# Optimization experiments

Measured on AMD Instinct MI355X. Metric: run time of the kernel, lower is better.

The kernel has to match this reference:

```python
import jax, jax.numpy as jnp
import numpy as np

F_IN = 128
HID = 256
OUT = 64
E = 500_000
NP_ALL = 304_096   # paper nodes: seed 4096 + hop1 100000 + hop2 200000
NP_H01 = 104_096   # paper nodes kept at layer 1 (seed + hop1)
NA_ALL = 154_096   # author nodes: 4096 + 50000 + 100000
NA_H01 = 54_096    # author nodes kept at layer 1


def setup_inputs() -> dict:
    key = jax.random.key(0)
    ks = iter(jax.random.split(key, 40))
    def nrm(shape, scale=0.05):
        return jax.random.normal(next(ks), shape, dtype=jnp.float32) * scale
    inp = {
        'x_paper': nrm((NP_ALL, F_IN), 1.0),
        'x_author': nrm((NA_ALL, F_IN), 1.0),
    }
    # per-layer, per-edge-type SAGEConv params: lin_l (W,b on aggregated msgs), lin_r (W, no bias, on dst)
    for li, fin in ((0, F_IN), (1, HID)):
        for rel in ('cites', 'writes', 'rev'):
            inp[f'l{li}_{rel}_Wl'] = nrm((fin, HID))
            inp[f'l{li}_{rel}_b'] = jnp.zeros((HID,), jnp.float32)
            inp[f'l{li}_{rel}_Wr'] = nrm((fin, HID))
    inp['lin_W'] = nrm((HID, OUT))
    inp['lin_b'] = jnp.zeros((OUT,), jnp.float32)
    # edge_index per edge type per sampled hop; hop-1 edges survive trimming at layer 1
    for name, hi in (('e_cites_h1', NP_H01), ('e_cites_h2', NP_ALL),
                     ('e_writes_h1', NA_H01), ('e_writes_h2', NA_ALL),
                     ('e_rev_h1', NA_H01), ('e_rev_h2', NA_ALL)):
        inp[name] = jax.random.randint(next(ks), (2, E), 0, hi, dtype=jnp.int32)
    return inp


def _sage(x_src, x_dst, edge, Wl, b, Wr):
    # SAGEConv: mean-aggregate neighbor features, lin_l(agg) + b + lin_r(x_dst)
    n_dst = x_dst.shape[0]
    msg = x_src[edge[0]]  # [E, F] gather
    s = jax.ops.segment_sum(msg, edge[1], num_segments=n_dst)
    cnt = jax.ops.segment_sum(jnp.ones((edge.shape[1],), x_src.dtype), edge[1], num_segments=n_dst)
    mean = s / jnp.maximum(cnt, 1.0)[:, None]  # 0 for isolated dst nodes (PyG mean)
    return mean @ Wl + b + x_dst @ Wr


def reference(x_paper, x_author,
              l0_cites_Wl, l0_cites_b, l0_cites_Wr,
              l0_writes_Wl, l0_writes_b, l0_writes_Wr,
              l0_rev_Wl, l0_rev_b, l0_rev_Wr,
              l1_cites_Wl, l1_cites_b, l1_cites_Wr,
              l1_writes_Wl, l1_writes_b, l1_writes_Wr,
              l1_rev_Wl, l1_rev_b, l1_rev_Wr,
              lin_W, lin_b,
              e_cites_h1, e_cites_h2, e_writes_h1, e_writes_h2, e_rev_h1, e_rev_h2):
    # ---- layer 0: no trimming -> all nodes, all (hop1+hop2) edges ----
    ec = jnp.concatenate([e_cites_h1, e_cites_h2], axis=1)
    ew = jnp.concatenate([e_writes_h1, e_writes_h2], axis=1)
    er = jnp.concatenate([e_rev_h1, e_rev_h2], axis=1)
    p = _sage(x_paper, x_paper, ec, l0_cites_Wl, l0_cites_b, l0_cites_Wr) \
      + _sage(x_author, x_paper, ew, l0_writes_Wl, l0_writes_b, l0_writes_Wr)
    a = _sage(x_paper, x_author, er, l0_rev_Wl, l0_rev_b, l0_rev_Wr)
    xp, xa = jax.nn.relu(p), jax.nn.relu(a)
    # ---- layer 1: trim_to_layer drops last hop nodes + hop-2 edges ----
    xp, xa = xp[:NP_H01], xa[:NA_H01]
    p = _sage(xp, xp, e_cites_h1, l1_cites_Wl, l1_cites_b, l1_cites_Wr) \
      + _sage(xa, xp, e_writes_h1, l1_writes_Wl, l1_writes_b, l1_writes_Wr)
    xp = jax.nn.relu(p)
    # final Linear on 'paper' features
    return xp @ lin_W + lin_b
```

## Files before the change

kernel.cpp:

```cpp
#include <hip/hip_runtime.h>

typedef unsigned short u16;
typedef unsigned int   u32;
typedef __bf16  bf16x8 __attribute__((ext_vector_type(8)));
typedef float   floatx4 __attribute__((ext_vector_type(4)));

#define NP_ALL 304096
#define NP_H01 104096
#define NA_ALL 154096
#define NA_H01 54096

#define SEG_C0 0
#define SEG_W0 104096
#define SEG_R0 208192
#define SEG_C1 262288
#define SEG_W1 366384
#define SCAN_N 470480
#define SCAN_NBLK 1838

__device__ __forceinline__ u16 f2bf(float f){
    u32 u = __float_as_uint(f);
    return (u16)((u + 0x7fffu + ((u>>16)&1u)) >> 16);
}
__device__ __forceinline__ float blo(u32 v){ return __uint_as_float(v<<16); }
__device__ __forceinline__ float bhi(u32 v){ return __uint_as_float(v & 0xFFFF0000u); }

__global__ void wcvt_k(u16* __restrict__ dst, const float* __restrict__ src, int n){
    int t = blockIdx.x*256 + threadIdx.x;
    if (t < n) dst[t] = f2bf(src[t]);
}
__global__ void wadd_k(u16* __restrict__ dst, const float* __restrict__ a, const float* __restrict__ b, int n){
    int t = blockIdx.x*256 + threadIdx.x;
    if (t < n) dst[t] = f2bf(a[t] + b[t]);
}
__global__ void bias_k(float* __restrict__ dst, const float* __restrict__ a, const float* __restrict__ b, int n){
    int t = blockIdx.x*256 + threadIdx.x;
    if (t < n) dst[t] = a[t] + (b ? b[t] : 0.0f);
}
__global__ void cvt2_k(u32* __restrict__ dst, const float* __restrict__ src, int n2){
    int t = blockIdx.x*256 + threadIdx.x;
    if (t >= n2) return;
    dst[t] = (u32)f2bf(src[2*t]) | ((u32)f2bf(src[2*t+1])<<16);
}
__global__ void repack_k(const u16* __restrict__ Wc, int K, int N, u16* __restrict__ Wp){
    int t = blockIdx.x*256 + threadIdx.x;
    int total = (K>>5)*(N>>4)*64;
    if (t >= total) return;
    int lane = t & 63;
    int nt = (t>>6) % (N>>4);
    int kt = (t>>6) / (N>>4);
    int n  = nt*16 + (lane & 15);
    int k0 = kt*32 + (lane>>4)*8;
    u16* dst = Wp + (size_t)t*8;
    #pragma unroll
    for (int j=0;j<8;j++) dst[j] = Wc[(size_t)(k0+j)*N + n];
}

__global__ void hist_k(const int* __restrict__ edst, int nE, int limit, int* __restrict__ deg){
    int t = blockIdx.x*256 + threadIdx.x;
    if (t >= nE) return;
    int d = edst[t];
    if (d < limit) atomicAdd(deg + d, 1);
}
__global__ void scan1_k(const int* __restrict__ deg, int* __restrict__ bsum){
    __shared__ int sm[256];
    int t = blockIdx.x*256 + threadIdx.x;
    sm[threadIdx.x] = (t < SCAN_N) ? deg[t] : 0;
    __syncthreads();
    for (int s=128; s>0; s>>=1){
        if (threadIdx.x < s) sm[threadIdx.x] += sm[threadIdx.x+s];
        __syncthreads();
    }
    if (threadIdx.x == 0) bsum[blockIdx.x] = sm[0];
}
__global__ void scan2_k(int* __restrict__ bsum, int n){
    __shared__ int sm[256];
    int chunk = (n + 255) >> 8;
    int st = threadIdx.x * chunk;
    int sum = 0;
    for (int i=0;i<chunk;i++){ int idx = st+i; if (idx < n) sum += bsum[idx]; }
    sm[threadIdx.x] = sum; __syncthreads();
    int acc = sum;
    for (int s=1; s<256; s<<=1){
        int t2 = (threadIdx.x >= s) ? sm[threadIdx.x - s] : 0;
        __syncthreads();
        acc += t2; sm[threadIdx.x] = acc;
        __syncthreads();
    }
    int excl = acc - sum;
    for (int i=0;i<chunk;i++){
        int idx = st+i;
        if (idx < n){ int v = bsum[idx]; bsum[idx] = excl; excl += v; }
    }
}
__global__ void scan3_k(const int* __restrict__ deg, const int* __restrict__ bsum,
                        int* __restrict__ rowptr, int* __restrict__ wp){
    __shared__ int sm[256];
    int t = blockIdx.x*256 + threadIdx.x;
    int v = (t < SCAN_N) ? deg[t] : 0;
    sm[threadIdx.x] = v; __syncthreads();
    int acc = v;
    for (int s=1; s<256; s<<=1){
        int t2 = (threadIdx.x >= s) ? sm[threadIdx.x - s] : 0;
        __syncthreads();
        acc += t2; sm[threadIdx.x] = acc;
        __syncthreads();
    }
    int excl = acc - v + bsum[blockIdx.x];
    if (t < SCAN_N){ rowptr[t] = excl; wp[t] = excl; }
    if (t == SCAN_N-1) rowptr[SCAN_N] = excl + v;
}
__global__ void fill_k(const int* __restrict__ esrc, const int* __restrict__ edst,
                       int nE, int limit, int* __restrict__ wp, int* __restrict__ pool){
    int t = blockIdx.x*256 + threadIdx.x;
    if (t >= nE) return;
    int d = edst[t];
    if (d >= limit) return;
    int p = atomicAdd(wp + d, 1);
    pool[p] = esrc[t];
}

template<int D>
__device__ __forceinline__ void gather_mean(
    const u16* __restrict__ srcl, size_t rstride,
    const int* __restrict__ rowptr, int seg, int d,
    const int* __restrict__ pool, u16* __restrict__ outl)
{
    int b = rowptr[seg + d], e = rowptr[seg + d + 1];
    float rc = 1.0f / (float)((e - b) > 1 ? (e - b) : 1);
    if (D == 128) {
        float a0=0,a1=0,c0=0,c1=0;
        int i = b;
        for (; i+1 < e; i += 2){
            int s0 = pool[i], s1 = pool[i+1];
            u32 v0 = *(const u32*)(srcl + (size_t)s0*rstride);
            u32 v1 = *(const u32*)(srcl + (size_t)s1*rstride);
            a0 += blo(v0); a1 += bhi(v0);
            c0 += blo(v1); c1 += bhi(v1);
        }
        if (i < e){
            int s0 = pool[i];
            u32 v0 = *(const u32*)(srcl + (size_t)s0*rstride);
            a0 += blo(v0); a1 += bhi(v0);
        }
        u32 lo = f2bf((a0+c0)*rc), hi = f2bf((a1+c1)*rc);
        *(u32*)outl = lo | (hi<<16);
    } else {
        float a0=0,a1=0,a2=0,a3=0,c0=0,c1=0,c2=0,c3=0;
        int i = b;
        for (; i+1 < e; i += 2){
            int s0 = pool[i], s1 = pool[i+1];
            uint2 v0 = *(const uint2*)(srcl + (size_t)s0*rstride);
            uint2 v1 = *(const uint2*)(srcl + (size_t)s1*rstride);
            a0 += blo(v0.x); a1 += bhi(v0.x); a2 += blo(v0.y); a3 += bhi(v0.y);
            c0 += blo(v1.x); c1 += bhi(v1.x); c2 += blo(v1.y); c3 += bhi(v1.y);
        }
        if (i < e){
            int s0 = pool[i];
            uint2 v0 = *(const uint2*)(srcl + (size_t)s0*rstride);
            a0 += blo(v0.x); a1 += bhi(v0.x); a2 += blo(v0.y); a3 += bhi(v0.y);
        }
        uint2 o;
        o.x = (u32)f2bf((a0+c0)*rc) | ((u32)f2bf((a1+c1)*rc)<<16);
        o.y = (u32)f2bf((a2+c2)*rc) | ((u32)f2bf((a3+c3)*rc)<<16);
        *(uint2*)outl = o;
    }
}


__global__ __launch_bounds__(256) void gAp_k(
    const u16* __restrict__ xpb, const u16* __restrict__ xab,
    const int* __restrict__ rowptr, const int* __restrict__ pool,
    u16* __restrict__ Ap)
{
    int gid = blockIdx.x*256 + threadIdx.x;
    int wid = gid >> 6, lane = gid & 63;
    if (wid >= NP_H01) return;
    const size_t SM = (size_t)NP_H01*64;
    size_t wofs = (size_t)wid*64 + 2*(lane&31);
    int hs = lane>>5;
    gather_mean<128>(xpb + 2*lane, 128, rowptr, SEG_C0, wid, pool, Ap + (size_t)(0+hs)*SM + wofs);
    gather_mean<128>(xab + 2*lane, 128, rowptr, SEG_W0, wid, pool, Ap + (size_t)(2+hs)*SM + wofs);
    u32 v = *(const u32*)(xpb + (size_t)wid*128 + 2*lane);
    *(u32*)(Ap + (size_t)(4+hs)*SM + wofs) = v;
}
__global__ __launch_bounds__(256) void gAa_k(
    const u16* __restrict__ xpb, const u16* __restrict__ xab,
    const int* __restrict__ rowptr, const int* __restrict__ pool,
    u16* __restrict__ Aa)
{
    int gid = blockIdx.x*256 + threadIdx.x;
    int wid = gid >> 6, lane = gid & 63;
    if (wid >= NA_H01) return;
    const size_t SM = (size_t)NA_H01*64;
    size_t wofs = (size_t)wid*64 + 2*(lane&31);
    int hs = lane>>5;
    gather_mean<128>(xpb + 2*lane, 128, rowptr, SEG_R0, wid, pool, Aa + (size_t)(0+hs)*SM + wofs);
    u32 v = *(const u32*)(xab + (size_t)wid*128 + 2*lane);
    *(u32*)(Aa + (size_t)(2+hs)*SM + wofs) = v;
}
__global__ __launch_bounds__(256) void gA1_k(
    const u16* __restrict__ A1src,
    const u16* __restrict__ xa,
    const int* __restrict__ rowptr, const int* __restrict__ pool,
    u16* __restrict__ A1)
{
    int gid = blockIdx.x*256 + threadIdx.x;
    int wid = gid >> 6, lane = gid & 63;
    if (wid >= NP_H01) return;
    const size_t SM = (size_t)NP_H01*64;
    int qs = lane>>4;
    size_t wofs = (size_t)wid*64 + 4*(lane&15);
    gather_mean<256>(A1src + (size_t)(8+qs)*SM + 4*(lane&15), 64,
                     rowptr, SEG_C1, wid, pool, A1 + (size_t)(0+qs)*SM + wofs);
    gather_mean<256>(xa + 4*lane, 256,
                     rowptr, SEG_W1, wid, pool, A1 + (size_t)(4+qs)*SM + wofs);
}

template<int WROWS, int WCOLS, int WMT, int WNT, bool RELU, bool F32OUT>
__global__ __launch_bounds__(256, 2) void gemm4_k(
    const u16* __restrict__ At, int M, int K,
    const u16* __restrict__ Wp, int nt16, const float* __restrict__ bias,
    void* __restrict__ C_, int ldc, int tileM, int colofs)
{
    constexpr int BNT  = WCOLS*WNT;
    constexpr int BM   = WROWS*WMT*16;
    constexpr int NSTG = 2*BNT;
    constexpr int PERW = NSTG/4;
    static_assert(2*WMT == 8, "vmcnt(8) literal assumes 8 A-loads per stage");
    __shared__ __align__(16) u16 ldsB[2*NSTG*512];

    int wave = threadIdx.x >> 6, lane = threadIdx.x & 63;
    int quad = lane >> 4, l15 = lane & 15;
    int wr = wave / WCOLS, wc = wave % WCOLS;
    int bm0 = blockIdx.x * BM;
    int ntb = blockIdx.y * BNT;
    const size_t SMS = (size_t)M*64;

    floatx4 acc[WMT][WNT];
    #pragma unroll
    for (int i=0;i<WMT;i++)
        #pragma unroll
        for (int j=0;j<WNT;j++) acc[i][j] = (floatx4){0.f,0.f,0.f,0.f};

    const u16* Abase[WMT];
    #pragma unroll
    for (int i=0;i<WMT;i++){
        int r = bm0 + (wr*WMT + i)*16 + l15;
        r = (r < M) ? r : (M-1);
        Abase[i] = At + (size_t)r*64 + quad*8;
    }

    int nstages = K >> 6;

    auto stage_issue = [&](int sn, int bufsel){
        #pragma unroll
        for (int i=0;i<PERW;i++){
            int g = wave*PERW + i;
            int ktl = g / BNT, ntl = g % BNT;
            const u16* gp = Wp + ((size_t)(sn*2+ktl)*nt16 + ntb + ntl)*512 + lane*8;
            u16* lp = ldsB + bufsel*(NSTG*512) + g*512 + lane*8;
            __builtin_amdgcn_global_load_lds(
                (const __attribute__((address_space(1))) void*)gp,
                (__attribute__((address_space(3))) void*)lp, 16, 0, 0);
        }
    };
    auto a_issue = [&](int sn, bf16x8 (&dst)[2][WMT]){
        #pragma unroll
        for (int ktl=0; ktl<2; ktl++)
            #pragma unroll
            for (int i=0;i<WMT;i++)
                dst[ktl][i] = *(const bf16x8*)(Abase[i] + (size_t)sn*SMS + ktl*32);
    };
    auto compute = [&](int bufsel, bf16x8 (&af)[2][WMT]){
        const u16* lb = ldsB + bufsel*(NSTG*512);
        #pragma unroll
        for (int ktl=0; ktl<2; ktl++){
            bf16x8 bfr[WNT];
            #pragma unroll
            for (int j=0;j<WNT;j++)
                bfr[j] = *(const bf16x8*)(lb + ((size_t)(ktl*BNT + wc*WNT + j)*64 + lane)*8);
            #pragma unroll
            for (int i=0;i<WMT;i++)
                #pragma unroll
                for (int j=0;j<WNT;j++)
                    acc[i][j] = __builtin_amdgcn_mfma_f32_16x16x32_bf16(af[ktl][i], bfr[j], acc[i][j], 0,0,0);
        }
    };

    bf16x8 aA[2][WMT], aB[2][WMT];
    stage_issue(0, 0);
    __builtin_amdgcn_sched_barrier(0);
    a_issue(0, aA);
    __builtin_amdgcn_sched_barrier(0);

    for (int s=0; s<nstages; s+=2){
        asm volatile("s_waitcnt lgkmcnt(0)" ::: "memory");
        asm volatile("s_waitcnt vmcnt(8)"  ::: "memory");
        __builtin_amdgcn_sched_barrier(0);
        __builtin_amdgcn_s_barrier();
        {
            int sn = s+1;
            stage_issue(sn, 1);
            __builtin_amdgcn_sched_barrier(0);
            a_issue(sn, aB);
            __builtin_amdgcn_sched_barrier(0);
            compute(0, aA);
        }
        asm volatile("s_waitcnt lgkmcnt(0)" ::: "memory");
        asm volatile("s_waitcnt vmcnt(8)"  ::: "memory");
        __builtin_amdgcn_sched_barrier(0);
        __builtin_amdgcn_s_barrier();
        {
            int sn = (s+2 < nstages) ? s+2 : 0;
            stage_issue(sn, 0);
            __builtin_amdgcn_sched_barrier(0);
            a_issue(sn, aA);
            __builtin_amdgcn_sched_barrier(0);
            compute(1, aB);
        }
    }
    asm volatile("s_waitcnt vmcnt(0)" ::: "memory");

    #pragma unroll
    for (int j=0;j<WNT;j++){
        int col = (ntb + wc*WNT + j)*16 + l15;
        float bv = bias[col];
        #pragma unroll
        for (int i=0;i<WMT;i++){
            int rbase = bm0 + (wr*WMT + i)*16 + quad*4;
            #pragma unroll
            for (int ii=0; ii<4; ii++){
                int row = rbase + ii;
                if (row < M){
                    float v = acc[i][j][ii] + bv;
                    if (RELU) v = fmaxf(v, 0.0f);
                    if (F32OUT) ((float*)C_)[(size_t)row*ldc + col] = v;
                    else if (tileM > 0){
                        int ct = col + colofs;
                        ((u16*)C_)[((size_t)(ct>>6)*tileM + row)*64 + (ct&63)] = f2bf(v);
                    } else {
                        ((u16*)C_)[(size_t)row*ldc + col] = f2bf(v);
                    }
                }
            }
        }
    }
}

extern "C" void kernel_launch(void* const* d_in, const int* in_sizes, int n_in,
                              void* d_out, int out_size, void* d_ws, size_t ws_size,
                              hipStream_t stream)
{
    const float* x_paper  = (const float*)d_in[0];
    const float* x_author = (const float*)d_in[1];
    const float* w_in[22];
    for (int i=0;i<22;i++) w_in[i] = (const float*)d_in[i];
    const int* e_c1 = (const int*)d_in[22]; int nE_c1 = in_sizes[22]/2;
    const int* e_c2 = (const int*)d_in[23]; int nE_c2 = in_sizes[23]/2;
    const int* e_w1 = (const int*)d_in[24]; int nE_w1 = in_sizes[24]/2;
    const int* e_w2 = (const int*)d_in[25]; int nE_w2 = in_sizes[25]/2;
    const int* e_r1 = (const int*)d_in[26]; int nE_r1 = in_sizes[26]/2;
    const int* e_r2 = (const int*)d_in[27]; int nE_r2 = in_sizes[27]/2;
    float* out = (float*)d_out;

    size_t off = 0;
    auto take = [&](size_t nb)->void* {
        void* p = (char*)d_ws + off;
        off = (off + nb + 255) & ~(size_t)255;
        return p;
    };
    u16*   A1  = (u16*)take((size_t)NP_H01*768*2);
    u16*   xa  = (u16*)take((size_t)NA_H01*256*2);
    u16*   Ap  = (u16*)take((size_t)NP_H01*384*2);
    u16*   Aa  = (u16*)take((size_t)NA_H01*256*2);
    int*   deg    = (int*)take((size_t)SCAN_N*4);
    int*   rowptr = (int*)take((size_t)(SCAN_N+1)*4);
    int*   wp     = (int*)take((size_t)SCAN_N*4);
    int*   bsum   = (int*)take((size_t)SCAN_NBLK*4);
    int*   pool   = (int*)take((size_t)4000000*4);
    u16* Wc0p = (u16*)take((size_t)384*256*2);
    u16* Wc0a = (u16*)take((size_t)256*256*2);
    u16* Wc1  = (u16*)take((size_t)768*256*2);
    u16* Wcf  = (u16*)take((size_t)256*64*2);
    u16* Wp0p = (u16*)take((size_t)384*256*2);
    u16* Wp0a = (u16*)take((size_t)256*256*2);
    u16* Wp1  = (u16*)take((size_t)768*256*2);
    u16* Wpf  = (u16*)take((size_t)256*64*2);
    float* b0p = (float*)take(256*4);
    float* b0a = (float*)take(256*4);
    float* b1  = (float*)take(256*4);
    float* bfin= (float*)take(64*4);

    u16* xpb = A1;
    u16* xab = A1 + (size_t)NP_ALL*128;
    u16* h1  = Ap;

    auto cdiv = [](long a, long b){ return (int)((a + b - 1)/b); };
    dim3 B(256);

    hipMemsetAsync(deg, 0, (size_t)SCAN_N*4, stream);

    wcvt_k<<<cdiv(32768,256),B,0,stream>>>(Wc0p,        w_in[2], 32768);
    wcvt_k<<<cdiv(32768,256),B,0,stream>>>(Wc0p+32768,  w_in[5], 32768);
    wadd_k<<<cdiv(32768,256),B,0,stream>>>(Wc0p+65536,  w_in[4], w_in[7], 32768);
    wcvt_k<<<cdiv(32768,256),B,0,stream>>>(Wc0a,        w_in[8], 32768);
    wcvt_k<<<cdiv(32768,256),B,0,stream>>>(Wc0a+32768,  w_in[10], 32768);
    wcvt_k<<<cdiv(65536,256),B,0,stream>>>(Wc1,         w_in[11], 65536);
    wcvt_k<<<cdiv(65536,256),B,0,stream>>>(Wc1+65536,   w_in[14], 65536);
    wadd_k<<<cdiv(65536,256),B,0,stream>>>(Wc1+131072,  w_in[13], w_in[16], 65536);
    wcvt_k<<<cdiv(16384,256),B,0,stream>>>(Wcf,         w_in[20], 16384);
    bias_k<<<1,B,0,stream>>>(b0p, w_in[3],  w_in[6],  256);
    bias_k<<<1,B,0,stream>>>(b0a, w_in[9],  nullptr,  256);
    bias_k<<<1,B,0,stream>>>(b1,  w_in[12], w_in[15], 256);
    bias_k<<<1,B,0,stream>>>(bfin,w_in[21], nullptr,  64);
    repack_k<<<cdiv(12288,256),B,0,stream>>>(Wc0p, 384, 256, Wp0p);
    repack_k<<<cdiv( 8192,256),B,0,stream>>>(Wc0a, 256, 256, Wp0a);
    repack_k<<<cdiv(24576,256),B,0,stream>>>(Wc1,  768, 256, Wp1);
    repack_k<<<cdiv( 2048,256),B,0,stream>>>(Wcf,  256,  64, Wpf);
    int n2p = NP_ALL*128/2, n2a = NA_ALL*128/2;
    cvt2_k<<<cdiv(n2p,256),B,0,stream>>>((u32*)xpb, x_paper,  n2p);
    cvt2_k<<<cdiv(n2a,256),B,0,stream>>>((u32*)xab, x_author, n2a);

    hist_k<<<cdiv(nE_c1,256),B,0,stream>>>(e_c1+nE_c1, nE_c1, NP_H01, deg+SEG_C0);
    hist_k<<<cdiv(nE_c2,256),B,0,stream>>>(e_c2+nE_c2, nE_c2, NP_H01, deg+SEG_C0);
    hist_k<<<cdiv(nE_w1,256),B,0,stream>>>(e_w1+nE_w1, nE_w1, NP_H01, deg+SEG_W0);
    hist_k<<<cdiv(nE_w2,256),B,0,stream>>>(e_w2+nE_w2, nE_w2, NP_H01, deg+SEG_W0);
    hist_k<<<cdiv(nE_r1,256),B,0,stream>>>(e_r1+nE_r1, nE_r1, NA_H01, deg+SEG_R0);
    hist_k<<<cdiv(nE_r2,256),B,0,stream>>>(e_r2+nE_r2, nE_r2, NA_H01, deg+SEG_R0);
    hist_k<<<cdiv(nE_c1,256),B,0,stream>>>(e_c1+nE_c1, nE_c1, NP_H01, deg+SEG_C1);
    hist_k<<<cdiv(nE_w1,256),B,0,stream>>>(e_w1+nE_w1, nE_w1, NP_H01, deg+SEG_W1);
    scan1_k<<<SCAN_NBLK,B,0,stream>>>(deg, bsum);
    scan2_k<<<1,B,0,stream>>>(bsum, SCAN_NBLK);
    scan3_k<<<SCAN_NBLK,B,0,stream>>>(deg, bsum, rowptr, wp);
    fill_k<<<cdiv(nE_c1,256),B,0,stream>>>(e_c1, e_c1+nE_c1, nE_c1, NP_H01, wp+SEG_C0, pool);
    fill_k<<<cdiv(nE_c2,256),B,0,stream>>>(e_c2, e_c2+nE_c2, nE_c2, NP_H01, wp+SEG_C0, pool);
    fill_k<<<cdiv(nE_w1,256),B,0,stream>>>(e_w1, e_w1+nE_w1, nE_w1, NP_H01, wp+SEG_W0, pool);
    fill_k<<<cdiv(nE_w2,256),B,0,stream>>>(e_w2, e_w2+nE_w2, nE_w2, NP_H01, wp+SEG_W0, pool);
    fill_k<<<cdiv(nE_r1,256),B,0,stream>>>(e_r1, e_r1+nE_r1, nE_r1, NA_H01, wp+SEG_R0, pool);
    fill_k<<<cdiv(nE_r2,256),B,0,stream>>>(e_r2, e_r2+nE_r2, nE_r2, NA_H01, wp+SEG_R0, pool);
    fill_k<<<cdiv(nE_c1,256),B,0,stream>>>(e_c1, e_c1+nE_c1, nE_c1, NP_H01, wp+SEG_C1, pool);
    fill_k<<<cdiv(nE_w1,256),B,0,stream>>>(e_w1, e_w1+nE_w1, nE_w1, NP_H01, wp+SEG_W1, pool);

    gAp_k<<<cdiv((long)NP_H01*64,256),B,0,stream>>>(xpb, xab, rowptr, pool, Ap);
    gAa_k<<<cdiv((long)NA_H01*64,256),B,0,stream>>>(xpb, xab, rowptr, pool, Aa);

    {
        dim3 g(cdiv(NP_H01,128), 2);
        gemm4_k<2,2,4,4,true,false><<<g,B,0,stream>>>(Ap, NP_H01, 384, Wp0p, 16, b0p, A1, 0, NP_H01, 512);
    }
    {
        dim3 g(cdiv(NA_H01,128), 2);
        gemm4_k<2,2,4,4,true,false><<<g,B,0,stream>>>(Aa, NA_H01, 256, Wp0a, 16, b0a, xa, 256, 0, 0);
    }

    gA1_k<<<cdiv((long)NP_H01*64,256),B,0,stream>>>(A1, xa, rowptr, pool, A1);

    {
        dim3 g(cdiv(NP_H01,128), 2);
        gemm4_k<2,2,4,4,true,false><<<g,B,0,stream>>>(A1, NP_H01, 768, Wp1, 16, b1, h1, 0, NP_H01, 0);
    }
    {
        dim3 g(cdiv(NP_H01,256), 1);
        gemm4_k<4,1,4,4,false,true><<<g,B,0,stream>>>(h1, NP_H01, 256, Wpf, 4, bfin, out, 64, 0, 0);
    }
}
```

Baseline: 1.265 ms.

## Replace LDS-staged B tiles with direct register loads in GEMM

The GEMM kernel no longer stages weight tiles through LDS with global_load_lds, manual waitcnt and block barriers. Each wave now loads its own A and B fragments from global memory straight into registers, with a one-step register double buffer. This drops LDS traffic and barriers but loads B redundantly across waves, leaning on cache. The occupancy hint in launch_bounds is also removed.

```diff
diff --git a/kernel.cpp b/kernel.cpp
--- a/kernel.cpp
+++ b/kernel.cpp
@@ -218,17 +218,13 @@
 }
 
 template<int WROWS, int WCOLS, int WMT, int WNT, bool RELU, bool F32OUT>
-__global__ __launch_bounds__(256, 2) void gemm4_k(
+__global__ __launch_bounds__(256) void gemm5_k(
     const u16* __restrict__ At, int M, int K,
     const u16* __restrict__ Wp, int nt16, const float* __restrict__ bias,
     void* __restrict__ C_, int ldc, int tileM, int colofs)
 {
-    constexpr int BNT  = WCOLS*WNT;
-    constexpr int BM   = WROWS*WMT*16;
-    constexpr int NSTG = 2*BNT;
-    constexpr int PERW = NSTG/4;
-    static_assert(2*WMT == 8, "vmcnt(8) literal assumes 8 A-loads per stage");
-    __shared__ __align__(16) u16 ldsB[2*NSTG*512];
+    constexpr int BNT = WCOLS*WNT;
+    constexpr int BM  = WROWS*WMT*16;
 
     int wave = threadIdx.x >> 6, lane = threadIdx.x & 63;
     int quad = lane >> 4, l15 = lane & 15;
@@ -250,77 +246,40 @@
         r = (r < M) ? r : (M-1);
         Abase[i] = At + (size_t)r*64 + quad*8;
     }
-
-    int nstages = K >> 6;
-
-    auto stage_issue = [&](int sn, int bufsel){
-        #pragma unroll
-        for (int i=0;i<PERW;i++){
-            int g = wave*PERW + i;
-            int ktl = g / BNT, ntl = g % BNT;
-            const u16* gp = Wp + ((size_t)(sn*2+ktl)*nt16 + ntb + ntl)*512 + lane*8;
-            u16* lp = ldsB + bufsel*(NSTG*512) + g*512 + lane*8;
-            __builtin_amdgcn_global_load_lds(
-                (const __attribute__((address_space(1))) void*)gp,
-                (__attribute__((address_space(3))) void*)lp, 16, 0, 0);
-        }
-    };
-    auto a_issue = [&](int sn, bf16x8 (&dst)[2][WMT]){
-        #pragma unroll
-        for (int ktl=0; ktl<2; ktl++)
-            #pragma unroll
-            for (int i=0;i<WMT;i++)
-                dst[ktl][i] = *(const bf16x8*)(Abase[i] + (size_t)sn*SMS + ktl*32);
-    };
-    auto compute = [&](int bufsel, bf16x8 (&af)[2][WMT]){
-        const u16* lb = ldsB + bufsel*(NSTG*512);
-        #pragma unroll
-        for (int ktl=0; ktl<2; ktl++){
-            bf16x8 bfr[WNT];
+    const u16* Bbase = Wp + ((size_t)(ntb + wc*WNT))*512 + lane*8;
+    const size_t BKT = (size_t)nt16*512;
+
+    int nk = K >> 5;
+
+    bf16x8 af[WMT], bf[WNT], afn[WMT], bfn[WNT];
+    #pragma unroll
+    for (int i=0;i<WMT;i++) af[i] = *(const bf16x8*)(Abase[i]);
+    #pragma unroll
+    for (int j=0;j<WNT;j++) bf[j] = *(const bf16x8*)(Bbase + (size_t)j*512);
+
+    for (int kt=0; kt+1<nk; kt++){
+        int kn = kt+1;
+        #pragma unroll
+        for (int i=0;i<WMT;i++)
+            afn[i] = *(const bf16x8*)(Abase[i] + (size_t)(kn>>1)*SMS + (kn&1)*32);
+        #pragma unroll
+        for (int j=0;j<WNT;j++)
+            bfn[j] = *(const bf16x8*)(Bbase + (size_t)kn*BKT + (size_t)j*512);
+        #pragma unroll
+        for (int i=0;i<WMT;i++)
             #pragma unroll
             for (int j=0;j<WNT;j++)
-                bfr[j] = *(const bf16x8*)(lb + ((size_t)(ktl*BNT + wc*WNT + j)*64 + lane)*8);
-            #pragma unroll
-            for (int i=0;i<WMT;i++)
-                #pragma unroll
-                for (int j=0;j<WNT;j++)
-                    acc[i][j] = __builtin_amdgcn_mfma_f32_16x16x32_bf16(af[ktl][i], bfr[j], acc[i][j], 0,0,0);
-        }
-    };
-
-    bf16x8 aA[2][WMT], aB[2][WMT];
-    stage_issue(0, 0);
-    __builtin_amdgcn_sched_barrier(0);
-    a_issue(0, aA);
-    __builtin_amdgcn_sched_barrier(0);
-
-    for (int s=0; s<nstages; s+=2){
-        asm volatile("s_waitcnt lgkmcnt(0)" ::: "memory");
-        asm volatile("s_waitcnt vmcnt(8)"  ::: "memory");
-        __builtin_amdgcn_sched_barrier(0);
-        __builtin_amdgcn_s_barrier();
-        {
-            int sn = s+1;
-            stage_issue(sn, 1);
-            __builtin_amdgcn_sched_barrier(0);
-            a_issue(sn, aB);
-            __builtin_amdgcn_sched_barrier(0);
-            compute(0, aA);
-        }
-        asm volatile("s_waitcnt lgkmcnt(0)" ::: "memory");
-        asm volatile("s_waitcnt vmcnt(8)"  ::: "memory");
-        __builtin_amdgcn_sched_barrier(0);
-        __builtin_amdgcn_s_barrier();
-        {
-            int sn = (s+2 < nstages) ? s+2 : 0;
-            stage_issue(sn, 0);
-            __builtin_amdgcn_sched_barrier(0);
-            a_issue(sn, aA);
-            __builtin_amdgcn_sched_barrier(0);
-            compute(1, aB);
-        }
-    }
-    asm volatile("s_waitcnt vmcnt(0)" ::: "memory");
+                acc[i][j] = __builtin_amdgcn_mfma_f32_16x16x32_bf16(af[i], bf[j], acc[i][j], 0,0,0);
+        #pragma unroll
+        for (int i=0;i<WMT;i++) af[i] = afn[i];
+        #pragma unroll
+        for (int j=0;j<WNT;j++) bf[j] = bfn[j];
+    }
+    #pragma unroll
+    for (int i=0;i<WMT;i++)
+        #pragma unroll
+        for (int j=0;j<WNT;j++)
+            acc[i][j] = __builtin_amdgcn_mfma_f32_16x16x32_bf16(af[i], bf[j], acc[i][j], 0,0,0);
 
     #pragma unroll
     for (int j=0;j<WNT;j++){
@@ -447,21 +406,21 @@
 
     {
         dim3 g(cdiv(NP_H01,128), 2);
-        gemm4_k<2,2,4,4,true,false><<<g,B,0,stream>>>(Ap, NP_H01, 384, Wp0p, 16, b0p, A1, 0, NP_H01, 512);
+        gemm5_k<2,2,4,4,true,false><<<g,B,0,stream>>>(Ap, NP_H01, 384, Wp0p, 16, b0p, A1, 0, NP_H01, 512);
     }
     {
         dim3 g(cdiv(NA_H01,128), 2);
-        gemm4_k<2,2,4,4,true,false><<<g,B,0,stream>>>(Aa, NA_H01, 256, Wp0a, 16, b0a, xa, 256, 0, 0);
+        gemm5_k<2,2,4,4,true,false><<<g,B,0,stream>>>(Aa, NA_H01, 256, Wp0a, 16, b0a, xa, 256, 0, 0);
     }
 
     gA1_k<<<cdiv((long)NP_H01*64,256),B,0,stream>>>(A1, xa, rowptr, pool, A1);
 
     {
         dim3 g(cdiv(NP_H01,128), 2);
-        gemm4_k<2,2,4,4,true,false><<<g,B,0,stream>>>(A1, NP_H01, 768, Wp1, 16, b1, h1, 0, NP_H01, 0);
+        gemm5_k<2,2,4,4,true,false><<<g,B,0,stream>>>(A1, NP_H01, 768, Wp1, 16, b1, h1, 0, NP_H01, 0);
     }
     {
         dim3 g(cdiv(NP_H01,256), 1);
-        gemm4_k<4,1,4,4,false,true><<<g,B,0,stream>>>(h1, NP_H01, 256, Wpf, 4, bfin, out, 64, 0, 0);
-    }
-}
+        gemm5_k<4,1,4,4,false,true><<<g,B,0,stream>>>(h1, NP_H01, 256, Wpf, 4, bfin, out, 64, 0, 0);
+    }
+}
```

New measurement: 1.267 ms. Within noise of the previous version (+0.2%).
